# Performance work log

Hardware: AMD Instinct MI355X
Metric: run time of the kernel (lower is better)

Reference implementation:

```python
import jax, jax.numpy as jnp
import numpy as np

B, S, D, H = 4, 2048, 768, 4
DH = D // H  # 192


def setup_inputs() -> dict:
    key = jax.random.key(0)
    ks = jax.random.split(key, 5)
    std = 1.0 / np.sqrt(D)
    return {
        "x": jax.random.normal(ks[0], (B, S, D), dtype=jnp.float32),
        "Wq": jax.random.normal(ks[1], (D, D), dtype=jnp.float32) * std,
        "Wk": jax.random.normal(ks[2], (D, D), dtype=jnp.float32) * std,
        "Wv": jax.random.normal(ks[3], (D, D), dtype=jnp.float32) * std,
        "Wo": jax.random.normal(ks[4], (D, D), dtype=jnp.float32) * std,
    }


def reference(x, Wq, Wk, Wv, Wo):
    b, s, d = x.shape
    # nn.Linear(bias=False): y = x @ W.T
    q = (x @ Wq.T).reshape(b, s, H, DH).transpose(0, 2, 1, 3)  # [B,H,S,DH]
    k = (x @ Wk.T).reshape(b, s, H, DH).transpose(0, 2, 1, 3)
    v = (x @ Wv.T).reshape(b, s, H, DH).transpose(0, 2, 1, 3)
    scale = jnp.sqrt(jnp.asarray(DH, dtype=q.dtype))
    logits = jnp.einsum("bhqd,bhkd->bhqk", q, k) / scale  # [B,H,S,S]
    causal = jnp.tril(jnp.ones((s, s), dtype=bool))
    logits = jnp.where(causal, logits, -jnp.inf)
    A = jax.nn.softmax(logits, axis=-1)
    preout = jnp.einsum("bhqk,bhkd->bhqd", A, v)  # [B,H,S,DH]
    # W_O = rearrange(Wo.T, '(h dh) dm -> h dh dm'); sum over heads == full Wo
    W_O = Wo.T.reshape(H, DH, D)
    out = jnp.einsum("bhsd,hdm->bsm", preout, W_O)  # [B,S,D]
    return out
```

## Files before the change

### kernel.cpp

```cpp
#include <hip/hip_runtime.h>
#include <hip/hip_bf16.h>

constexpr int CB = 4, CS = 2048, CD = 768, CH = 4, CDH = 192;
constexpr int CM = CB * CS;

typedef float f32x4 __attribute__((ext_vector_type(4)));
typedef float fx4 __attribute__((ext_vector_type(4)));
typedef __bf16 bx8 __attribute__((ext_vector_type(8)));
typedef unsigned short u16;
typedef u16 u16x8 __attribute__((ext_vector_type(8)));
typedef u16 u16x4 __attribute__((ext_vector_type(4)));

static __device__ __forceinline__ u16 f32_bf16(float f) {
  unsigned u = __builtin_bit_cast(unsigned, f);
  u += 0x7FFFu + ((u >> 16) & 1u);
  return (u16)(u >> 16);
}
static __device__ __forceinline__ float bf16_f32(u16 v) {
  return __builtin_bit_cast(float, (unsigned)v << 16);
}

static __device__ __forceinline__ f32x4 mfma16(bx8 a, bx8 b, f32x4 c) {
  return __builtin_amdgcn_mfma_f32_16x16x32_bf16(a, b, c, 0, 0, 0);
}

static __device__ __forceinline__ void load_lds16(const u16* g, u16* l) {
  __builtin_amdgcn_global_load_lds(
      (const __attribute__((address_space(1))) unsigned int*)g,
      (__attribute__((address_space(3))) unsigned int*)l, 16, 0, 0);
}

__global__ void __launch_bounds__(256) convert_all(
    const float* __restrict__ x, const float* __restrict__ wq,
    const float* __restrict__ wk, const float* __restrict__ wv,
    const float* __restrict__ wo, u16* __restrict__ xb, u16* __restrict__ wqb,
    u16* __restrict__ wkb, u16* __restrict__ wvb, u16* __restrict__ wob) {
  const float* srcs[5] = {x, wq, wk, wv, wo};
  u16* dsts[5] = {xb, wqb, wkb, wvb, wob};
  const int n4s[5] = {CM * CD / 4, CD * CD / 4, CD * CD / 4, CD * CD / 4,
                      CD * CD / 4};
  const int gsz = gridDim.x * blockDim.x;
  const int gid = blockIdx.x * blockDim.x + threadIdx.x;
#pragma unroll
  for (int sg = 0; sg < 5; ++sg) {
    const fx4* src = (const fx4*)srcs[sg];
    u16* dst = dsts[sg];
    const int n4 = n4s[sg];
    for (int i = gid; i < n4; i += gsz) {
      fx4 v = src[i];
      u16x4 o;
      o[0] = f32_bf16(v[0]);
      o[1] = f32_bf16(v[1]);
      o[2] = f32_bf16(v[2]);
      o[3] = f32_bf16(v[3]);
      *(u16x4*)&dst[(size_t)i * 4] = o;
    }
  }
}

template <bool OUT_BF16>
__global__ void __launch_bounds__(256) gemm_bt(
    const u16* __restrict__ A, const u16* __restrict__ Bw0,
    const u16* __restrict__ Bw1, const u16* __restrict__ Bw2,
    void* __restrict__ C0, void* __restrict__ C1, void* __restrict__ C2,
    int M, int N, int K) {
  constexpr int LDK = 72;
  __shared__ u16 As[128][LDK];
  __shared__ u16 Bs[128][LDK];
  const int z = blockIdx.z;
  const u16* Bw = (z == 0) ? Bw0 : ((z == 1) ? Bw1 : Bw2);
  void* Cv = (z == 0) ? C0 : ((z == 1) ? C1 : C2);
  const int m0 = blockIdx.x * 128;
  const int n0 = blockIdx.y * 128;
  const int tid = threadIdx.x;
  const int wave = tid >> 6, lane = tid & 63;
  const int wr = wave >> 1, wc = wave & 1;
  const int lr = lane & 15, lhi = lane >> 4;

  f32x4 acc[4][4];
  const f32x4 zero = {0.f, 0.f, 0.f, 0.f};
#pragma unroll
  for (int i = 0; i < 4; ++i)
#pragma unroll
    for (int j = 0; j < 4; ++j) acc[i][j] = zero;

  u16x8 areg[4], breg[4];
  auto ldregs = [&](int kk) {
#pragma unroll
    for (int r = 0; r < 4; ++r) {
      const int id = tid + r * 256;
      const int row = id >> 3, ch = id & 7;
      areg[r] = *(const u16x8*)&A[(size_t)(m0 + row) * K + kk + ch * 8];
      breg[r] = *(const u16x8*)&Bw[(size_t)(n0 + row) * K + kk + ch * 8];
    }
  };

  ldregs(0);
  for (int kk = 0; kk < K; kk += 64) {
    __syncthreads();
#pragma unroll
    for (int r = 0; r < 4; ++r) {
      const int id = tid + r * 256;
      const int row = id >> 3, ch = id & 7;
      *(u16x8*)&As[row][ch * 8] = areg[r];
      *(u16x8*)&Bs[row][ch * 8] = breg[r];
    }
    if (kk + 64 < K) ldregs(kk + 64);
    __syncthreads();
#pragma unroll
    for (int ks = 0; ks < 2; ++ks) {
      bx8 af[4], bf[4];
#pragma unroll
      for (int mf = 0; mf < 4; ++mf)
        af[mf] = *(const bx8*)&As[wr * 64 + mf * 16 + lr][ks * 32 + lhi * 8];
#pragma unroll
      for (int nf = 0; nf < 4; ++nf)
        bf[nf] = *(const bx8*)&Bs[wc * 64 + nf * 16 + lr][ks * 32 + lhi * 8];
      __builtin_amdgcn_s_setprio(1);
#pragma unroll
      for (int mf = 0; mf < 4; ++mf)
#pragma unroll
        for (int nf = 0; nf < 4; ++nf)
          acc[mf][nf] = mfma16(af[mf], bf[nf], acc[mf][nf]);
      __builtin_amdgcn_s_setprio(0);
    }
  }
#pragma unroll
  for (int mf = 0; mf < 4; ++mf)
#pragma unroll
    for (int nf = 0; nf < 4; ++nf)
#pragma unroll
      for (int r = 0; r < 4; ++r) {
        const int row = m0 + wr * 64 + mf * 16 + lhi * 4 + r;
        const int col = n0 + wc * 64 + nf * 16 + lr;
        if constexpr (OUT_BF16)
          ((u16*)Cv)[(size_t)row * N + col] = f32_bf16(acc[mf][nf][r]);
        else
          ((float*)Cv)[(size_t)row * N + col] = acc[mf][nf][r];
      }
}

#define PKE(q, k0, k1, p)                                               \
  ((unsigned)(q) | ((unsigned)(k0) << 4) | ((unsigned)(k1) << 9) |      \
   ((unsigned)((p) + 1) << 15))
__device__ const unsigned FA_TBL[32] = {
    PKE(10, 0, 11, 0),   PKE(10, 11, 22, 1),  PKE(15, 0, 11, 2),
    PKE(15, 11, 22, 3),  PKE(4, 0, 10, -1),   PKE(9, 0, 10, 4),
    PKE(9, 10, 20, 5),   PKE(13, 0, 10, 6),   PKE(14, 0, 10, 7),
    PKE(14, 10, 20, 8),  PKE(14, 20, 30, 9),  PKE(15, 22, 32, 10),
    PKE(8, 0, 9, 11),    PKE(8, 9, 18, 12),   PKE(12, 0, 9, 13),
    PKE(12, 9, 18, 14),  PKE(0, 0, 2, -1),    PKE(1, 0, 4, -1),
    PKE(2, 0, 6, -1),    PKE(5, 0, 6, 15),    PKE(5, 6, 12, 16),
    PKE(6, 0, 7, 17),    PKE(6, 7, 14, 18),   PKE(3, 0, 8, -1),
    PKE(7, 0, 8, 19),    PKE(7, 8, 16, 20),   PKE(11, 0, 8, 21),
    PKE(11, 8, 16, 22),  PKE(11, 16, 24, 23), PKE(12, 18, 26, 24),
    PKE(13, 10, 19, 25), PKE(13, 19, 28, 26)};

__global__ void __launch_bounds__(256, 2) flash_attn(
    const u16* __restrict__ Qg, const u16* __restrict__ Kg,
    const u16* __restrict__ Vg, u16* __restrict__ Og, u16* __restrict__ pO,
    float* __restrict__ pML) {
  __shared__ u16 Ks[12288];
  __shared__ u16 Vs[12288];
  __shared__ u16 Ps[4][32][72];
  const int i0_ = blockIdx.x;
  const int xcd = i0_ & 7;
  const int r_ = i0_ >> 3;
  const int bh = xcd * 2 + (r_ & 1);
  const int s = r_ >> 1;
  const unsigned e = FA_TBL[s];
  const int q128 = (int)(e & 15u);
  const int kt0 = (int)((e >> 4) & 31u);
  const int kt1 = (int)((e >> 9) & 63u);
  const int pidx = (int)((e >> 15) & 63u) - 1;
  const int b = bh >> 2, h = bh & 3;
  const int tid = threadIdx.x;
  const int wave = tid >> 6, lane = tid & 63;
  const int lr = lane & 15, lhi = lane >> 4;
  const size_t base_elem = ((size_t)b * CS) * CD + (size_t)h * CDH;
  constexpr float scale = 0.07216878364870323f;
  const f32x4 zero = {0.f, 0.f, 0.f, 0.f};

  int kOff[6], vOff[6];
#pragma unroll
  for (int r = 0; r < 6; ++r) {
    const int p = tid + r * 256;
    {
      const int k = p / 24, c16 = p - k * 24;
      const unsigned swz = ((unsigned)(c16 * 16)) ^ ((unsigned)((k & 7) << 4));
      kOff[r] = k * CD + (int)(swz >> 1);
    }
    {
      const int blk = p >> 3, kq = (p >> 1) & 3, dh = p & 1;
      const int kk = ((blk & 15) << 2) + kq;
      const int d = ((blk >> 4) << 4) + dh * 8;
      vOff[r] = kk * CD + d;
    }
  }
  const unsigned vlds0 =
      (unsigned)(unsigned long long)(__attribute__((address_space(3)))
                                         u16*)&Vs[0];

  float m_run[2] = {-INFINITY, -INFINITY};
  float l_run[2] = {0.f, 0.f};
  f32x4 acc[2][12];
#pragma unroll
  for (int qg = 0; qg < 2; ++qg)
#pragma unroll
    for (int nf = 0; nf < 12; ++nf) acc[qg][nf] = zero;

  bx8 qf[2][6];
  {
    const int qrow0 = q128 * 128 + wave * 32;
#pragma unroll
    for (int qg = 0; qg < 2; ++qg) {
      const size_t qoff = base_elem + (size_t)(qrow0 + qg * 16 + lr) * CD;
#pragma unroll
      for (int c = 0; c < 6; ++c)
        qf[qg][c] = *(const bx8*)&Qg[qoff + c * 32 + lhi * 8];
    }
  }

  for (int kt = kt0; kt < kt1; ++kt) {
    __syncthreads();
    {
      const u16* kg = Kg + base_elem + (size_t)(kt * 64) * CD;
      const u16* vg = Vg + base_elem + (size_t)(kt * 64) * CD;
#pragma unroll
      for (int r = 0; r < 6; ++r)
        load_lds16(kg + kOff[r], &Ks[(size_t)(tid + r * 256) * 8]);
#pragma unroll
      for (int r = 0; r < 6; ++r)
        load_lds16(vg + vOff[r], &Vs[(size_t)(tid + r * 256) * 8]);
    }
    __syncthreads();

    const int k0 = kt * 64;
    const bool diag = (kt >= 2 * q128);
    f32x4 st[2][4];
#pragma unroll
    for (int qg = 0; qg < 2; ++qg)
#pragma unroll
      for (int mf = 0; mf < 4; ++mf) st[qg][mf] = zero;
    __builtin_amdgcn_s_setprio(1);
#pragma unroll
    for (int c = 0; c < 6; ++c)
#pragma unroll
      for (int mf = 0; mf < 4; ++mf) {
        const int row = mf * 16 + lr;
        const unsigned off =
            ((unsigned)(c * 64 + lhi * 16)) ^ ((unsigned)((row & 7) << 4));
        const bx8 kf =
            *(const bx8*)((const char*)Ks + (size_t)row * 384 + off);
        st[0][mf] = mfma16(kf, qf[0][c], st[0][mf]);
        st[1][mf] = mfma16(kf, qf[1][c], st[1][mf]);
      }
    __builtin_amdgcn_s_setprio(0);

#pragma unroll
    for (int qg = 0; qg < 2; ++qg) {
      const int qg_row = q128 * 128 + wave * 32 + qg * 16 + lr;
      float pvv[16];
#pragma unroll
      for (int mf = 0; mf < 4; ++mf)
#pragma unroll
        for (int r = 0; r < 4; ++r) {
          float sv = st[qg][mf][r] * scale;
          if (diag && (k0 + mf * 16 + lhi * 4 + r > qg_row)) sv = -INFINITY;
          pvv[mf * 4 + r] = sv;
        }
      float mx = pvv[0];
#pragma unroll
      for (int tt = 1; tt < 16; ++tt) mx = fmaxf(mx, pvv[tt]);
      mx = fmaxf(mx, __shfl_xor(mx, 16, 64));
      mx = fmaxf(mx, __shfl_xor(mx, 32, 64));
      const bool skip = __all(mx - m_run[qg] <= 8.0f);
      if (!skip) {
        const float mnew = fmaxf(m_run[qg], mx);
        const float alpha = __expf(m_run[qg] - mnew);
        float afr[4];
#pragma unroll
        for (int r = 0; r < 4; ++r)
          afr[r] = __shfl(alpha, lhi * 4 + r, 64);
#pragma unroll
        for (int nf = 0; nf < 12; ++nf)
#pragma unroll
          for (int r = 0; r < 4; ++r) acc[qg][nf][r] *= afr[r];
        l_run[qg] *= alpha;
        m_run[qg] = mnew;
      }
      float rs = 0.f;
#pragma unroll
      for (int tt = 0; tt < 16; ++tt) {
        const float ev = __expf(pvv[tt] - m_run[qg]);
        pvv[tt] = ev;
        rs += ev;
      }
      rs += __shfl_xor(rs, 16, 64);
      rs += __shfl_xor(rs, 32, 64);
      l_run[qg] += rs;
#pragma unroll
      for (int mf = 0; mf < 4; ++mf)
#pragma unroll
        for (int rp = 0; rp < 2; ++rp) {
          const unsigned w0 = f32_bf16(pvv[mf * 4 + rp * 2]);
          const unsigned w1 = f32_bf16(pvv[mf * 4 + rp * 2 + 1]);
          *(unsigned*)&Ps[wave][qg * 16 + lr][mf * 16 + lhi * 4 + rp * 2] =
              w0 | (w1 << 16);
        }
    }

    const bx8 pf[2][2] = {
        {*(const bx8*)&Ps[wave][lr][lhi * 8],
         *(const bx8*)&Ps[wave][lr][32 + lhi * 8]},
        {*(const bx8*)&Ps[wave][16 + lr][lhi * 8],
         *(const bx8*)&Ps[wave][16 + lr][32 + lhi * 8]}};
#pragma unroll
    for (int gg = 0; gg < 3; ++gg) {
      u16x4 tl[4][2], th[4][2];
#pragma unroll
      for (int q4 = 0; q4 < 4; ++q4)
#pragma unroll
        for (int c2 = 0; c2 < 2; ++c2) {
          const int nf = gg * 4 + q4;
          const unsigned va =
              vlds0 + (unsigned)((nf * 16 + c2 * 8 + lhi * 2) * 128 + lr * 8);
          asm volatile("ds_read_b64_tr_b16 %0, %2\n\t"
                       "ds_read_b64_tr_b16 %1, %2 offset:128"
                       : "=&v"(tl[q4][c2]), "=&v"(th[q4][c2])
                       : "v"(va));
        }
      asm volatile("s_waitcnt lgkmcnt(0)" ::: "memory");
      __builtin_amdgcn_sched_barrier(0);
      __builtin_amdgcn_s_setprio(1);
#pragma unroll
      for (int q4 = 0; q4 < 4; ++q4)
#pragma unroll
        for (int c2 = 0; c2 < 2; ++c2) {
          const int nf = gg * 4 + q4;
          const u16x8 vv = __builtin_shufflevector(tl[q4][c2], th[q4][c2], 0,
                                                   1, 2, 3, 4, 5, 6, 7);
          const bx8 vb = __builtin_bit_cast(bx8, vv);
          acc[0][nf] = mfma16(pf[0][c2], vb, acc[0][nf]);
          acc[1][nf] = mfma16(pf[1][c2], vb, acc[1][nf]);
        }
      __builtin_amdgcn_s_setprio(0);
    }
  }

  if (pidx < 0) {
#pragma unroll
    for (int qg = 0; qg < 2; ++qg)
#pragma unroll
      for (int r = 0; r < 4; ++r) {
        const float lb = __shfl(l_run[qg], lhi * 4 + r, 64);
        const float linv = 1.0f / lb;
        const size_t orow =
            base_elem +
            (size_t)(q128 * 128 + wave * 32 + qg * 16 + lhi * 4 + r) * CD;
#pragma unroll
        for (int nf = 0; nf < 12; ++nf)
          Og[orow + nf * 16 + lr] = f32_bf16(acc[qg][nf][r] * linv);
      }
  } else {
    const int pbase = bh * 27 + pidx;
    if (lhi == 0) {
#pragma unroll
      for (int qg = 0; qg < 2; ++qg) {
        pML[pbase * 256 + wave * 32 + qg * 16 + lr] = m_run[qg];
        pML[pbase * 256 + 128 + wave * 32 + qg * 16 + lr] = l_run[qg];
      }
    }
#pragma unroll
    for (int qg = 0; qg < 2; ++qg)
#pragma unroll
      for (int r = 0; r < 4; ++r) {
        const float lb = __shfl(l_run[qg], lhi * 4 + r, 64);
        const float linv = 1.0f / lb;
        u16* dst = pO + ((size_t)pbase * 128 + wave * 32 + qg * 16 +
                         lhi * 4 + r) *
                            192;
#pragma unroll
        for (int nf = 0; nf < 12; ++nf)
          dst[nf * 16 + lr] = f32_bf16(acc[qg][nf][r] * linv);
      }
  }
}

#define CBE(n, p0, p1, p2) \
  ((unsigned)(n) | ((unsigned)(p0) << 2) | ((unsigned)(p1) << 8) | \
   ((unsigned)(p2) << 14))
__device__ const unsigned CB_TBL[11] = {
    CBE(2, 15, 16, 0), CBE(2, 17, 18, 0), CBE(2, 19, 20, 0),
    CBE(2, 11, 12, 0), CBE(2, 4, 5, 0),   CBE(2, 0, 1, 0),
    CBE(3, 21, 22, 23), CBE(3, 13, 14, 24), CBE(3, 6, 25, 26),
    CBE(3, 7, 8, 9),    CBE(3, 2, 3, 10)};

__global__ void __launch_bounds__(256) combine_qt(
    const u16* __restrict__ pO, const float* __restrict__ pML,
    u16* __restrict__ Og) {
  const int cb = blockIdx.x;
  const int bh = cb / 11, qi = cb % 11;
  const int q128 = qi + 5;
  const unsigned e = CB_TBL[qi];
  const int n = (int)(e & 3u);
  const int pid0 = (int)((e >> 2) & 63u);
  const int pid1 = (int)((e >> 8) & 63u);
  const int pid2 = (int)((e >> 14) & 63u);
  const int b = bh >> 2, h = bh & 3;
  const int tid = threadIdx.x;
  const int row = tid >> 1, half = tid & 1;
  float m[3], l[3];
  const int pids[3] = {pid0, pid1, pid2};
  for (int i = 0; i < n; ++i) {
    m[i] = pML[(bh * 27 + pids[i]) * 256 + row];
    l[i] = pML[(bh * 27 + pids[i]) * 256 + 128 + row];
  }
  float M = m[0];
  for (int i = 1; i < n; ++i) M = fmaxf(M, m[i]);
  float w[3], wsum = 0.f;
  for (int i = 0; i < n; ++i) {
    w[i] = l[i] * __expf(m[i] - M);
    wsum += w[i];
  }
  const float inv = 1.0f / wsum;
  const size_t obase =
      ((size_t)b * CS + (size_t)q128 * 128 + row) * CD + h * CDH + half * 96;
#pragma unroll
  for (int c = 0; c < 12; ++c) {
    float a8[8] = {0.f, 0.f, 0.f, 0.f, 0.f, 0.f, 0.f, 0.f};
    for (int i = 0; i < n; ++i) {
      const u16x8 v = *(const u16x8*)&pO[((size_t)(bh * 27 + pids[i]) * 128 +
                                          row) *
                                             192 +
                                         half * 96 + c * 8];
      const float f = w[i] * inv;
#pragma unroll
      for (int j = 0; j < 8; ++j) a8[j] += f * bf16_f32(v[j]);
    }
    u16x8 o;
#pragma unroll
    for (int j = 0; j < 8; ++j) o[j] = f32_bf16(a8[j]);
    *(u16x8*)&Og[obase + c * 8] = o;
  }
}

extern "C" void kernel_launch(void* const* d_in, const int* in_sizes, int n_in,
                              void* d_out, int out_size, void* d_ws,
                              size_t ws_size, hipStream_t stream) {
  (void)in_sizes;
  (void)n_in;
  (void)out_size;
  (void)ws_size;
  const float* x = (const float*)d_in[0];
  const float* wq = (const float*)d_in[1];
  const float* wk = (const float*)d_in[2];
  const float* wv = (const float*)d_in[3];
  const float* wo = (const float*)d_in[4];
  float* out = (float*)d_out;
  char* ws = (char*)d_ws;
  const size_t big = (size_t)CM * CD * 2;
  const size_t wsz = (size_t)CD * CD * 2;
  u16* xb = (u16*)ws;
  u16* qb = (u16*)(ws + big);
  u16* kb = (u16*)(ws + 2 * big);
  u16* vb = (u16*)(ws + 3 * big);
  u16* wqb = (u16*)(ws + 4 * big);
  u16* wkb = (u16*)(ws + 4 * big + wsz);
  u16* wvb = (u16*)(ws + 4 * big + 2 * wsz);
  u16* wob = (u16*)(ws + 4 * big + 3 * wsz);
  u16* pob = xb;
  u16* pO = (u16*)d_out;
  float* pML = (float*)((char*)d_out + (size_t)16 * 27 * 128 * 192 * 2);

  convert_all<<<dim3(2048), dim3(256), 0, stream>>>(x, wq, wk, wv, wo, xb, wqb,
                                                    wkb, wvb, wob);
  gemm_bt<true><<<dim3(64, 6, 3), dim3(256), 0, stream>>>(
      xb, wqb, wkb, wvb, (void*)qb, (void*)kb, (void*)vb, CM, CD, CD);
  flash_attn<<<dim3(512), dim3(256), 0, stream>>>(qb, kb, vb, pob, pO, pML);
  combine_qt<<<dim3(176), dim3(256), 0, stream>>>(pO, pML, pob);
  gemm_bt<false><<<dim3(64, 6, 1), dim3(256), 0, stream>>>(
      pob, wob, wob, wob, (void*)out, (void*)out, (void*)out, CM, CD, CD);
}
```

Baseline: 153.0 us.

## Restructure flash attention to 8 waves of 16 rows with register-staged K/V prefetch

The flash attention kernel goes from 4 waves each handling 32 query rows to 8 waves each handling 16 rows (512 threads). Each wave now holds half the accumulators and Q fragments, which lowers register pressure and raises occupancy. The direct global-to-LDS loads are replaced by register prefetch of the next K/V tile, overlapped with the current tile's compute. Barriers become raw s_barrier with explicit lgkmcnt waits, and this also applies to the GEMM. Softmax max and sum reductions become tree-shaped. The trade-off is less MFMA reuse of each K/V fragment per wave and more LDS reads of K and V across waves.

```diff
diff --git a/kernel.cpp b/kernel.cpp
--- a/kernel.cpp
+++ b/kernel.cpp
@@ -24,10 +24,14 @@
   return __builtin_amdgcn_mfma_f32_16x16x32_bf16(a, b, c, 0, 0, 0);
 }
 
-static __device__ __forceinline__ void load_lds16(const u16* g, u16* l) {
-  __builtin_amdgcn_global_load_lds(
-      (const __attribute__((address_space(1))) unsigned int*)g,
-      (__attribute__((address_space(3))) unsigned int*)l, 16, 0, 0);
+static __device__ __forceinline__ void bar_bare() {
+  __builtin_amdgcn_s_barrier();
+  __builtin_amdgcn_sched_barrier(0);
+}
+static __device__ __forceinline__ void bar_lgkm() {
+  asm volatile("s_waitcnt lgkmcnt(0)" ::: "memory");
+  __builtin_amdgcn_s_barrier();
+  __builtin_amdgcn_sched_barrier(0);
 }
 
 __global__ void __launch_bounds__(256) convert_all(
@@ -97,7 +101,7 @@
 
   ldregs(0);
   for (int kk = 0; kk < K; kk += 64) {
-    __syncthreads();
+    bar_bare();
 #pragma unroll
     for (int r = 0; r < 4; ++r) {
       const int id = tid + r * 256;
@@ -106,7 +110,7 @@
       *(u16x8*)&Bs[row][ch * 8] = breg[r];
     }
     if (kk + 64 < K) ldregs(kk + 64);
-    __syncthreads();
+    bar_lgkm();
 #pragma unroll
     for (int ks = 0; ks < 2; ++ks) {
       bx8 af[4], bf[4];
@@ -156,13 +160,13 @@
     PKE(11, 8, 16, 22),  PKE(11, 16, 24, 23), PKE(12, 18, 26, 24),
     PKE(13, 10, 19, 25), PKE(13, 19, 28, 26)};
 
-__global__ void __launch_bounds__(256, 2) flash_attn(
+__global__ void __launch_bounds__(512, 4) flash_attn(
     const u16* __restrict__ Qg, const u16* __restrict__ Kg,
     const u16* __restrict__ Vg, u16* __restrict__ Og, u16* __restrict__ pO,
     float* __restrict__ pML) {
   __shared__ u16 Ks[12288];
   __shared__ u16 Vs[12288];
-  __shared__ u16 Ps[4][32][72];
+  __shared__ u16 Ps[8][16][72];
   const int i0_ = blockIdx.x;
   const int xcd = i0_ & 7;
   const int r_ = i0_ >> 3;
@@ -181,10 +185,10 @@
   constexpr float scale = 0.07216878364870323f;
   const f32x4 zero = {0.f, 0.f, 0.f, 0.f};
 
-  int kOff[6], vOff[6];
-#pragma unroll
-  for (int r = 0; r < 6; ++r) {
-    const int p = tid + r * 256;
+  int kOff[3], vOff[3];
+#pragma unroll
+  for (int r = 0; r < 3; ++r) {
+    const int p = tid + r * 512;
     {
       const int k = p / 24, c16 = p - k * 24;
       const unsigned swz = ((unsigned)(c16 * 16)) ^ ((unsigned)((k & 7) << 4));
@@ -201,47 +205,49 @@
       (unsigned)(unsigned long long)(__attribute__((address_space(3)))
                                          u16*)&Vs[0];
 
-  float m_run[2] = {-INFINITY, -INFINITY};
-  float l_run[2] = {0.f, 0.f};
-  f32x4 acc[2][12];
-#pragma unroll
-  for (int qg = 0; qg < 2; ++qg)
-#pragma unroll
-    for (int nf = 0; nf < 12; ++nf) acc[qg][nf] = zero;
-
-  bx8 qf[2][6];
+  float m_run = -INFINITY, l_run = 0.f;
+  f32x4 acc[12];
+#pragma unroll
+  for (int nf = 0; nf < 12; ++nf) acc[nf] = zero;
+
+  bx8 qf[6];
   {
-    const int qrow0 = q128 * 128 + wave * 32;
-#pragma unroll
-    for (int qg = 0; qg < 2; ++qg) {
-      const size_t qoff = base_elem + (size_t)(qrow0 + qg * 16 + lr) * CD;
-#pragma unroll
-      for (int c = 0; c < 6; ++c)
-        qf[qg][c] = *(const bx8*)&Qg[qoff + c * 32 + lhi * 8];
-    }
-  }
+    const size_t qoff =
+        base_elem + (size_t)(q128 * 128 + wave * 16 + lr) * CD;
+#pragma unroll
+    for (int c = 0; c < 6; ++c)
+      qf[c] = *(const bx8*)&Qg[qoff + c * 32 + lhi * 8];
+  }
+
+  u16x8 kreg[3], vreg[3];
+  auto ldregs = [&](int kt) {
+    const u16* kg = Kg + base_elem + (size_t)(kt * 64) * CD;
+    const u16* vg = Vg + base_elem + (size_t)(kt * 64) * CD;
+#pragma unroll
+    for (int r = 0; r < 3; ++r) {
+      kreg[r] = *(const u16x8*)&kg[kOff[r]];
+      vreg[r] = *(const u16x8*)&vg[vOff[r]];
+    }
+  };
+
+  const int qg_row = q128 * 128 + wave * 16 + lr;
+  ldregs(kt0);
 
   for (int kt = kt0; kt < kt1; ++kt) {
-    __syncthreads();
-    {
-      const u16* kg = Kg + base_elem + (size_t)(kt * 64) * CD;
-      const u16* vg = Vg + base_elem + (size_t)(kt * 64) * CD;
-#pragma unroll
-      for (int r = 0; r < 6; ++r)
-        load_lds16(kg + kOff[r], &Ks[(size_t)(tid + r * 256) * 8]);
-#pragma unroll
-      for (int r = 0; r < 6; ++r)
-        load_lds16(vg + vOff[r], &Vs[(size_t)(tid + r * 256) * 8]);
-    }
-    __syncthreads();
+    bar_bare();
+#pragma unroll
+    for (int r = 0; r < 3; ++r) {
+      *(u16x8*)&Ks[(size_t)(tid + r * 512) * 8] = kreg[r];
+      *(u16x8*)&Vs[(size_t)(tid + r * 512) * 8] = vreg[r];
+    }
+    if (kt + 1 < kt1) ldregs(kt + 1);
+    bar_lgkm();
 
     const int k0 = kt * 64;
     const bool diag = (kt >= 2 * q128);
-    f32x4 st[2][4];
-#pragma unroll
-    for (int qg = 0; qg < 2; ++qg)
-#pragma unroll
-      for (int mf = 0; mf < 4; ++mf) st[qg][mf] = zero;
+    f32x4 st[4];
+#pragma unroll
+    for (int mf = 0; mf < 4; ++mf) st[mf] = zero;
     __builtin_amdgcn_s_setprio(1);
 #pragma unroll
     for (int c = 0; c < 6; ++c)
@@ -252,69 +258,64 @@
             ((unsigned)(c * 64 + lhi * 16)) ^ ((unsigned)((row & 7) << 4));
         const bx8 kf =
             *(const bx8*)((const char*)Ks + (size_t)row * 384 + off);
-        st[0][mf] = mfma16(kf, qf[0][c], st[0][mf]);
-        st[1][mf] = mfma16(kf, qf[1][c], st[1][mf]);
+        st[mf] = mfma16(kf, qf[c], st[mf]);
       }
     __builtin_amdgcn_s_setprio(0);
 
-#pragma unroll
-    for (int qg = 0; qg < 2; ++qg) {
-      const int qg_row = q128 * 128 + wave * 32 + qg * 16 + lr;
-      float pvv[16];
-#pragma unroll
-      for (int mf = 0; mf < 4; ++mf)
-#pragma unroll
-        for (int r = 0; r < 4; ++r) {
-          float sv = st[qg][mf][r] * scale;
-          if (diag && (k0 + mf * 16 + lhi * 4 + r > qg_row)) sv = -INFINITY;
-          pvv[mf * 4 + r] = sv;
-        }
-      float mx = pvv[0];
-#pragma unroll
-      for (int tt = 1; tt < 16; ++tt) mx = fmaxf(mx, pvv[tt]);
-      mx = fmaxf(mx, __shfl_xor(mx, 16, 64));
-      mx = fmaxf(mx, __shfl_xor(mx, 32, 64));
-      const bool skip = __all(mx - m_run[qg] <= 8.0f);
-      if (!skip) {
-        const float mnew = fmaxf(m_run[qg], mx);
-        const float alpha = __expf(m_run[qg] - mnew);
-        float afr[4];
-#pragma unroll
-        for (int r = 0; r < 4; ++r)
-          afr[r] = __shfl(alpha, lhi * 4 + r, 64);
-#pragma unroll
-        for (int nf = 0; nf < 12; ++nf)
-#pragma unroll
-          for (int r = 0; r < 4; ++r) acc[qg][nf][r] *= afr[r];
-        l_run[qg] *= alpha;
-        m_run[qg] = mnew;
+    float pvv[16];
+#pragma unroll
+    for (int mf = 0; mf < 4; ++mf)
+#pragma unroll
+      for (int r = 0; r < 4; ++r) {
+        float sv = st[mf][r] * scale;
+        if (diag && (k0 + mf * 16 + lhi * 4 + r > qg_row)) sv = -INFINITY;
+        pvv[mf * 4 + r] = sv;
       }
-      float rs = 0.f;
-#pragma unroll
-      for (int tt = 0; tt < 16; ++tt) {
-        const float ev = __expf(pvv[tt] - m_run[qg]);
-        pvv[tt] = ev;
-        rs += ev;
+    float t8[8];
+#pragma unroll
+    for (int i = 0; i < 8; ++i) t8[i] = fmaxf(pvv[2 * i], pvv[2 * i + 1]);
+#pragma unroll
+    for (int i = 0; i < 4; ++i) t8[i] = fmaxf(t8[2 * i], t8[2 * i + 1]);
+    float mx = fmaxf(fmaxf(t8[0], t8[1]), fmaxf(t8[2], t8[3]));
+    mx = fmaxf(mx, __shfl_xor(mx, 16, 64));
+    mx = fmaxf(mx, __shfl_xor(mx, 32, 64));
+    const bool skip = __all(mx - m_run <= 8.0f);
+    if (!skip) {
+      const float mnew = fmaxf(m_run, mx);
+      const float alpha = __expf(m_run - mnew);
+      float afr[4];
+#pragma unroll
+      for (int r = 0; r < 4; ++r) afr[r] = __shfl(alpha, lhi * 4 + r, 64);
+#pragma unroll
+      for (int nf = 0; nf < 12; ++nf)
+#pragma unroll
+        for (int r = 0; r < 4; ++r) acc[nf][r] *= afr[r];
+      l_run *= alpha;
+      m_run = mnew;
+    }
+#pragma unroll
+    for (int tt = 0; tt < 16; ++tt) pvv[tt] = __expf(pvv[tt] - m_run);
+    float s8[8];
+#pragma unroll
+    for (int i = 0; i < 8; ++i) s8[i] = pvv[2 * i] + pvv[2 * i + 1];
+#pragma unroll
+    for (int i = 0; i < 4; ++i) s8[i] = s8[2 * i] + s8[2 * i + 1];
+    float rs = (s8[0] + s8[1]) + (s8[2] + s8[3]);
+    rs += __shfl_xor(rs, 16, 64);
+    rs += __shfl_xor(rs, 32, 64);
+    l_run += rs;
+
+#pragma unroll
+    for (int mf = 0; mf < 4; ++mf)
+#pragma unroll
+      for (int rp = 0; rp < 2; ++rp) {
+        const unsigned w0 = f32_bf16(pvv[mf * 4 + rp * 2]);
+        const unsigned w1 = f32_bf16(pvv[mf * 4 + rp * 2 + 1]);
+        *(unsigned*)&Ps[wave][lr][mf * 16 + lhi * 4 + rp * 2] =
+            w0 | (w1 << 16);
       }
-      rs += __shfl_xor(rs, 16, 64);
-      rs += __shfl_xor(rs, 32, 64);
-      l_run[qg] += rs;
-#pragma unroll
-      for (int mf = 0; mf < 4; ++mf)
-#pragma unroll
-        for (int rp = 0; rp < 2; ++rp) {
-          const unsigned w0 = f32_bf16(pvv[mf * 4 + rp * 2]);
-          const unsigned w1 = f32_bf16(pvv[mf * 4 + rp * 2 + 1]);
-          *(unsigned*)&Ps[wave][qg * 16 + lr][mf * 16 + lhi * 4 + rp * 2] =
-              w0 | (w1 << 16);
-        }
-    }
-
-    const bx8 pf[2][2] = {
-        {*(const bx8*)&Ps[wave][lr][lhi * 8],
-         *(const bx8*)&Ps[wave][lr][32 + lhi * 8]},
-        {*(const bx8*)&Ps[wave][16 + lr][lhi * 8],
-         *(const bx8*)&Ps[wave][16 + lr][32 + lhi * 8]}};
+    const bx8 pf0 = *(const bx8*)&Ps[wave][lr][lhi * 8];
+    const bx8 pf1 = *(const bx8*)&Ps[wave][lr][32 + lhi * 8];
 #pragma unroll
     for (int gg = 0; gg < 3; ++gg) {
       u16x4 tl[4][2], th[4][2];
@@ -340,9 +341,8 @@
           const int nf = gg * 4 + q4;
           const u16x8 vv = __builtin_shufflevector(tl[q4][c2], th[q4][c2], 0,
                                                    1, 2, 3, 4, 5, 6, 7);
-          const bx8 vb = __builtin_bit_cast(bx8, vv);
-          acc[0][nf] = mfma16(pf[0][c2], vb, acc[0][nf]);
-          acc[1][nf] = mfma16(pf[1][c2], vb, acc[1][nf]);
+          acc[nf] = mfma16(c2 == 0 ? pf0 : pf1, __builtin_bit_cast(bx8, vv),
+                           acc[nf]);
         }
       __builtin_amdgcn_s_setprio(0);
     }
@@ -350,40 +350,32 @@
 
   if (pidx < 0) {
 #pragma unroll
-    for (int qg = 0; qg < 2; ++qg)
-#pragma unroll
-      for (int r = 0; r < 4; ++r) {
-        const float lb = __shfl(l_run[qg], lhi * 4 + r, 64);
-        const float linv = 1.0f / lb;
-        const size_t orow =
-            base_elem +
-            (size_t)(q128 * 128 + wave * 32 + qg * 16 + lhi * 4 + r) * CD;
-#pragma unroll
-        for (int nf = 0; nf < 12; ++nf)
-          Og[orow + nf * 16 + lr] = f32_bf16(acc[qg][nf][r] * linv);
-      }
+    for (int r = 0; r < 4; ++r) {
+      const float lb = __shfl(l_run, lhi * 4 + r, 64);
+      const float linv = 1.0f / lb;
+      const size_t orow =
+          base_elem +
+          (size_t)(q128 * 128 + wave * 16 + lhi * 4 + r) * CD;
+#pragma unroll
+      for (int nf = 0; nf < 12; ++nf)
+        Og[orow + nf * 16 + lr] = f32_bf16(acc[nf][r] * linv);
+    }
   } else {
     const int pbase = bh * 27 + pidx;
     if (lhi == 0) {
-#pragma unroll
-      for (int qg = 0; qg < 2; ++qg) {
-        pML[pbase * 256 + wave * 32 + qg * 16 + lr] = m_run[qg];
-        pML[pbase * 256 + 128 + wave * 32 + qg * 16 + lr] = l_run[qg];
-      }
-    }
-#pragma unroll
-    for (int qg = 0; qg < 2; ++qg)
-#pragma unroll
-      for (int r = 0; r < 4; ++r) {
-        const float lb = __shfl(l_run[qg], lhi * 4 + r, 64);
-        const float linv = 1.0f / lb;
-        u16* dst = pO + ((size_t)pbase * 128 + wave * 32 + qg * 16 +
-                         lhi * 4 + r) *
-                            192;
-#pragma unroll
-        for (int nf = 0; nf < 12; ++nf)
-          dst[nf * 16 + lr] = f32_bf16(acc[qg][nf][r] * linv);
-      }
+      pML[pbase * 256 + wave * 16 + lr] = m_run;
+      pML[pbase * 256 + 128 + wave * 16 + lr] = l_run;
+    }
+#pragma unroll
+    for (int r = 0; r < 4; ++r) {
+      const float lb = __shfl(l_run, lhi * 4 + r, 64);
+      const float linv = 1.0f / lb;
+      u16* dst =
+          pO + ((size_t)pbase * 128 + wave * 16 + lhi * 4 + r) * 192;
+#pragma unroll
+      for (int nf = 0; nf < 12; ++nf)
+        dst[nf * 16 + lr] = f32_bf16(acc[nf][r] * linv);
+    }
   }
 }
 
@@ -477,7 +469,7 @@
                                                     wkb, wvb, wob);
   gemm_bt<true><<<dim3(64, 6, 3), dim3(256), 0, stream>>>(
       xb, wqb, wkb, wvb, (void*)qb, (void*)kb, (void*)vb, CM, CD, CD);
-  flash_attn<<<dim3(512), dim3(256), 0, stream>>>(qb, kb, vb, pob, pO, pML);
+  flash_attn<<<dim3(512), dim3(512), 0, stream>>>(qb, kb, vb, pob, pO, pML);
   combine_qt<<<dim3(176), dim3(256), 0, stream>>>(pO, pML, pob);
   gemm_bt<false><<<dim3(64, 6, 1), dim3(256), 0, stream>>>(
       pob, wob, wob, wob, (void*)out, (void*)out, (void*)out, CM, CD, CD);
```

Result: slower. 269.2 us (+75.9%).
